# Optimization experiments

Hardware: AMD Instinct MI355X
Metric: run time of the kernel (lower is better)

Reference implementation:

```python
import jax, jax.numpy as jnp
import numpy as np

N = 8192
D = 128
NUM_INSTANCES = 8  # samples per class (balanced PK batch)
ALPHA = 50.0
BASE = 1.0


def setup_inputs() -> dict:
    key = jax.random.key(0)
    k1, = jax.random.split(key, 1)
    x = jax.random.normal(k1, (N, D), dtype=jnp.float32)
    # L2-normalize so pairwise dists ~ sqrt(2) and exp(alpha*(1-d)) stays finite in fp32
    inputs = x / jnp.linalg.norm(x, axis=1, keepdims=True)
    targets = (jnp.arange(N) // NUM_INSTANCES).astype(jnp.int64)
    return {"inputs": inputs, "targets": targets}


def _euclidean_dist(x):
    sq = jnp.sum(x * x, axis=1)  # [n]
    d2 = sq[:, None] + sq[None, :] - 2.0 * (x @ x.T)  # [n, n]
    return jnp.sqrt(jnp.clip(d2, 1e-12, None))


def reference(inputs, targets):
    n = inputs.shape[0]
    dist = _euclidean_dist(inputs)                      # [n, n]
    same = targets[:, None] == targets[None, :]         # [n, n] bool
    eye = jnp.eye(n, dtype=bool)
    pos_mask = same & ~eye                              # positives, excluding self
    neg_mask = ~same                                    # negatives

    e = jnp.exp(ALPHA * (BASE - dist))                  # [n, n]
    pos_logit = jnp.sum(jnp.where(pos_mask, e, 0.0), axis=1)        # [n]
    neg_logit = jnp.sum(jnp.where(neg_mask, e, 0.0), axis=1) * 0.5  # [n]
    loss = jnp.mean(-jnp.log(pos_logit / (pos_logit + neg_logit)))

    pos_d = jnp.sum(jnp.where(pos_mask, dist, 0.0)) / jnp.sum(pos_mask)
    neg_d = jnp.sum(jnp.where(neg_mask, dist, 0.0)) / jnp.sum(neg_mask)
    prec = jnp.float32(1.0)  # err is always 0 in the original code
    return (loss, prec, pos_d, neg_d)
```

## Files before the change

kernel.cpp:

```cpp
#include <hip/hip_runtime.h>

#define NN 8192
#define DD 128
#define C2 72.13475204444817f
#define LN2 0.6931471805599453f
#define NTILE 64
#define NTRI 2080
#define DPAD 2112

typedef __attribute__((ext_vector_type(8))) __bf16 bf16x8;
typedef __attribute__((ext_vector_type(4))) float f32x4;

#if __has_builtin(__builtin_amdgcn_exp2f)
#define EXP2F(x) __builtin_amdgcn_exp2f(x)
#else
#define EXP2F(x) exp2f(x)
#endif
#if __has_builtin(__builtin_amdgcn_sqrtf)
#define SQRTF(x) __builtin_amdgcn_sqrtf(x)
#else
#define SQRTF(x) sqrtf(x)
#endif
#if __has_builtin(__builtin_amdgcn_logf)
#define LOG2F(x) __builtin_amdgcn_logf(x)
#else
#define LOG2F(x) log2f(x)
#endif

__device__ __forceinline__ unsigned short f2bf(float f) {
  unsigned u = __float_as_uint(f);
  u += 0x7FFFu + ((u >> 16) & 1u);
  return (unsigned short)(u >> 16);
}

__device__ __forceinline__ void gload_lds16(const void* g, void* l) {
  __builtin_amdgcn_global_load_lds(
      (const __attribute__((address_space(1))) void*)g,
      (__attribute__((address_space(3))) void*)l, 16, 0, 0);
}

__global__ __launch_bounds__(512) void prep_pos_kernel(
    const float* __restrict__ x, unsigned short* __restrict__ xbf,
    float* __restrict__ sq, float* __restrict__ pos_e,
    float* __restrict__ pos_d, float* __restrict__ dpart,
    float* __restrict__ accs, unsigned* __restrict__ cnt) {
  int w = threadIdx.x >> 6;
  int lane = threadIdx.x & 63;
  int i = blockIdx.x * 8 + w;

  __shared__ float xs[8][128];
  __shared__ float sqs[8];

  const float* xr = x + (size_t)i * DD;
  float a = xr[lane], b = xr[lane + 64];
  xs[w][lane] = a;
  xs[w][lane + 64] = b;

  float s = __fmaf_rn(a, a, b * b);
#pragma unroll
  for (int m = 32; m; m >>= 1) s += __shfl_xor(s, m, 64);
  if (lane == 0) {
    sq[i] = s;
    sqs[w] = s;
  }
  unsigned short* o = xbf + (size_t)i * DD;
  int t1 = lane >> 3, e1 = lane & 7;
  o[((t1 ^ w) << 3) + e1] = f2bf(a);
  o[64 + ((t1 ^ w) << 3) + e1] = f2bf(b);
  if (blockIdx.x == 0) {
    if (threadIdx.x < 32) dpart[NTRI + threadIdx.x] = 0.f;
    if (threadIdx.x == 32) {
      accs[0] = 0.f;
      accs[1] = 0.f;
      accs[2] = 0.f;
    }
    if (threadIdx.x == 33) cnt[0] = 0u;
  }

  __syncthreads();
  float sqi = sqs[w];
  float pe = 0.f, pd = 0.f;
  for (int j = 0; j < 8; ++j) {
    if (j == w) continue;
    float dot = __fmaf_rn(a, xs[j][lane], b * xs[j][lane + 64]);
#pragma unroll
    for (int m = 32; m; m >>= 1) dot += __shfl_xor(dot, m, 64);
    float d2 = fmaxf(__fmaf_rn(-2.f, dot, sqi + sqs[j]), 1e-12f);
    float dist = SQRTF(d2);
    pe += EXP2F(__fmaf_rn(dist, -C2, C2));
    pd += dist;
  }
  if (lane == 0) {
    pos_e[i] = pe;
    pos_d[i] = pd;
  }
}

__global__ __launch_bounds__(256, 2) void tile_kernel(
    const unsigned short* __restrict__ xbf, const float* __restrict__ sq,
    float* __restrict__ part, float* __restrict__ dpart) {
  int lane = threadIdx.x & 63;
  int wave = threadIdx.x >> 6;
  int q = lane >> 4, c = lane & 15;

  int b = blockIdx.x;
  int tr = (int)((129.0f - SQRTF(16641.0f - 8.0f * (float)b)) * 0.5f);
  while (tr > 0 && tr * (129 - tr) / 2 > b) --tr;
  while ((tr + 1) * (128 - tr) / 2 <= b) ++tr;
  int tc = tr + (b - tr * (129 - tr) / 2);
  bool diag = (tr == tc);

  __shared__ char panel[65536];
  __shared__ float rowsum[128];
  __shared__ float colsum[128];
  __shared__ float partd[4];

  {
    const char* gA = (const char*)xbf + (size_t)tr * 32768;
    const char* gB = (const char*)xbf + (size_t)tc * 32768;
    int goff = wave * 1024 + lane * 16;
    char* lA = panel + wave * 1024;
    char* lB = panel + 32768 + wave * 1024;
#pragma unroll
    for (int t = 0; t < 8; ++t) {
      gload_lds16(gA + t * 4096 + goff, lA + t * 4096);
      gload_lds16(gB + t * 4096 + goff, lB + t * 4096);
    }
  }

  if (threadIdx.x < 128)
    rowsum[threadIdx.x] = 0.f;
  else
    colsum[threadIdx.x - 128] = 0.f;

  int I0 = tr * 128 + (wave >> 1) * 64;
  int J0 = tc * 128 + (wave & 1) * 64;

  float sqi[16];
#pragma unroll
  for (int rb = 0; rb < 4; ++rb)
#pragma unroll
    for (int r = 0; r < 4; ++r)
      sqi[rb * 4 + r] = sq[I0 + rb * 16 + q * 4 + r];
  float sqj[4];
#pragma unroll
  for (int cb = 0; cb < 4; ++cb) sqj[cb] = sq[J0 + cb * 16 + c];

  f32x4 acc[4][4];
#pragma unroll
  for (int rb = 0; rb < 4; ++rb)
#pragma unroll
    for (int cb = 0; cb < 4; ++cb) acc[rb][cb] = (f32x4){0.f, 0.f, 0.f, 0.f};

  __syncthreads();

  {
    int swz = (c & 7) << 4;
    const char* pa = panel + (wave >> 1) * 16384 + c * 256;
    const char* pb = panel + 32768 + (wave & 1) * 16384 + c * 256;
#pragma unroll
    for (int ks = 0; ks < 4; ++ks) {
      int koff = (ks * 64 + q * 16) ^ swz;
      bf16x8 ar[4], br[4];
#pragma unroll
      for (int rb = 0; rb < 4; ++rb)
        ar[rb] = *(const bf16x8*)(pa + rb * 4096 + koff);
#pragma unroll
      for (int cb = 0; cb < 4; ++cb)
        br[cb] = *(const bf16x8*)(pb + cb * 4096 + koff);
#pragma unroll
      for (int rb = 0; rb < 4; ++rb)
#pragma unroll
        for (int cb = 0; cb < 4; ++cb)
          acc[rb][cb] = __builtin_amdgcn_mfma_f32_16x16x32_bf16(
              ar[rb], br[cb], acc[rb][cb], 0, 0, 0);
    }
  }

  float tote[16];
#pragma unroll
  for (int k = 0; k < 16; ++k) tote[k] = 0.f;
  float pcol[4] = {0.f, 0.f, 0.f, 0.f};
  float totd = 0.f;

#pragma unroll
  for (int rb = 0; rb < 4; ++rb) {
#pragma unroll
    for (int cb = 0; cb < 4; ++cb) {
      bool diagTile = (I0 + rb * 16) == (J0 + cb * 16);
#pragma unroll
      for (int r = 0; r < 4; ++r) {
        float d2 = fmaxf(
            __fmaf_rn(-2.f, acc[rb][cb][r], sqi[rb * 4 + r] + sqj[cb]),
            1e-12f);
        float dist = SQRTF(d2);
        float ex = EXP2F(__fmaf_rn(dist, -C2, C2));
        if (diagTile && (q * 4 + r) == c) {
          ex = 0.f;
          dist = 0.f;
        }
        tote[rb * 4 + r] += ex;
        pcol[cb] += ex;
        totd += dist;
      }
    }
  }

#pragma unroll
  for (int k = 0; k < 16; ++k) {
    float v = tote[k];
    v += __shfl_xor(v, 1, 64);
    v += __shfl_xor(v, 2, 64);
    v += __shfl_xor(v, 4, 64);
    v += __shfl_xor(v, 8, 64);
    tote[k] = v;
  }
  int woff = (wave >> 1) * 64;
  if (c == 0) {
#pragma unroll
    for (int rb = 0; rb < 4; ++rb)
#pragma unroll
      for (int r = 0; r < 4; ++r)
        atomicAdd(&rowsum[woff + rb * 16 + q * 4 + r], tote[rb * 4 + r]);
  }

  if (!diag) {
    int coff = (wave & 1) * 64;
#pragma unroll
    for (int cb = 0; cb < 4; ++cb) {
      float cs = pcol[cb];
      cs += __shfl_xor(cs, 16, 64);
      cs += __shfl_xor(cs, 32, 64);
      if (q == 0) atomicAdd(&colsum[coff + cb * 16 + c], cs);
    }
  }

#pragma unroll
  for (int m = 32; m; m >>= 1) totd += __shfl_xor(totd, m, 64);
  if (lane == 0) partd[wave] = totd;
  __syncthreads();

  size_t rslot = ((size_t)tr * NTILE + tc) * 128;
  size_t cslot = ((size_t)tc * NTILE + tr) * 128;
  int t = threadIdx.x;
  if (t < 128)
    part[rslot + t] = rowsum[t];
  else if (!diag)
    part[cslot + (t - 128)] = colsum[t - 128];
  if (t == 0) {
    float s = partd[0] + partd[1] + partd[2] + partd[3];
    dpart[blockIdx.x] = diag ? s : 2.f * s;
  }
}

__global__ __launch_bounds__(128) void fin_kernel(
    const float* __restrict__ part, const float* __restrict__ dpart,
    const float* __restrict__ pos_e, const float* __restrict__ pos_d,
    float* accs, unsigned* cnt, float* __restrict__ out) {
  int a = blockIdx.x, c = threadIdx.x;
  const float* pa = part + (size_t)a * NTILE * 128 + c;
  float tot = 0.f;
#pragma unroll
  for (int t = 0; t < 64; ++t) tot += pa[(size_t)t * 128];
  int i = a * 128 + c;
  float p = pos_e[i];
  float denom = __fmaf_rn(0.5f, tot - p, p);
  float lsum = LOG2F(denom) - LOG2F(p);
  float pdsum = pos_d[i];
  float ds = (c < 33) ? dpart[a * 33 + c] : 0.f;

  __shared__ float s1[128], s2[128], s3[128];
  s1[c] = lsum;
  s2[c] = pdsum;
  s3[c] = ds;
  __syncthreads();
  for (int w = 64; w; w >>= 1) {
    if (c < w) {
      s1[c] += s1[c + w];
      s2[c] += s2[c + w];
      s3[c] += s3[c + w];
    }
    __syncthreads();
  }
  if (c == 0) {
    atomicAdd(&accs[0], s1[0]);
    atomicAdd(&accs[1], s2[0]);
    atomicAdd(&accs[2], s3[0]);
    __threadfence();
    unsigned old = atomicAdd(cnt, 1u);
    if (old == 63u) {
      float L = atomicAdd(&accs[0], 0.f);
      float PD = atomicAdd(&accs[1], 0.f);
      float DS = atomicAdd(&accs[2], 0.f);
      out[0] = L * LN2 / (float)NN;
      out[1] = 1.0f;
      out[2] = PD / (float)(NN * 7);
      out[3] = (DS - PD) / ((float)NN * 8184.f);
    }
  }
}

extern "C" void kernel_launch(void* const* d_in, const int* in_sizes, int n_in,
                              void* d_out, int out_size, void* d_ws,
                              size_t ws_size, hipStream_t stream) {
  const float* x = (const float*)d_in[0];
  float* out = (float*)d_out;
  char* ws = (char*)d_ws;

  unsigned short* xbf = (unsigned short*)ws;
  float* sq = (float*)(ws + (size_t)NN * DD * 2);
  float* pos_e = sq + NN;
  float* pos_d = pos_e + NN;
  float* part = pos_d + NN;
  float* dpart = part + (size_t)NTILE * NTILE * 128;
  float* accs = dpart + DPAD;
  unsigned* cnt = (unsigned*)(accs + 3);

  prep_pos_kernel<<<NN / 8, 512, 0, stream>>>(x, xbf, sq, pos_e, pos_d, dpart,
                                              accs, cnt);
  tile_kernel<<<NTRI, 256, 0, stream>>>(xbf, sq, part, dpart);
  fin_kernel<<<64, 128, 0, stream>>>(part, dpart, pos_e, pos_d, accs, cnt,
                                     out);
}
```

Before: 102.9 us.

## Make tile kernel persistent over paired triangle rows with double-buffered B panels

The tile kernel now launches 512 blocks instead of 2080. Each block pairs row p with row 63-p so the triangular work is balanced, keeps both A row panels resident, and loops over a contiguous range of column tiles. It double-buffers the B panel, prefetching the next tile while computing the current one. LDS atomics are replaced by per-wave slots, and the distance partials are accumulated in registers with one dpart per block. This amortises A loads and launch/prologue cost, but uses about 128KB of LDS, so occupancy drops to one block per CU and there are two block barriers per tile.

```diff
diff --git a/kernel.cpp b/kernel.cpp
--- a/kernel.cpp
+++ b/kernel.cpp
@@ -5,8 +5,6 @@
 #define C2 72.13475204444817f
 #define LN2 0.6931471805599453f
 #define NTILE 64
-#define NTRI 2080
-#define DPAD 2112
 
 typedef __attribute__((ext_vector_type(8))) __bf16 bf16x8;
 typedef __attribute__((ext_vector_type(4))) float f32x4;
@@ -42,8 +40,8 @@
 __global__ __launch_bounds__(512) void prep_pos_kernel(
     const float* __restrict__ x, unsigned short* __restrict__ xbf,
     float* __restrict__ sq, float* __restrict__ pos_e,
-    float* __restrict__ pos_d, float* __restrict__ dpart,
-    float* __restrict__ accs, unsigned* __restrict__ cnt) {
+    float* __restrict__ pos_d, float* __restrict__ accs,
+    unsigned* __restrict__ cnt) {
   int w = threadIdx.x >> 6;
   int lane = threadIdx.x & 63;
   int i = blockIdx.x * 8 + w;
@@ -68,13 +66,12 @@
   o[((t1 ^ w) << 3) + e1] = f2bf(a);
   o[64 + ((t1 ^ w) << 3) + e1] = f2bf(b);
   if (blockIdx.x == 0) {
-    if (threadIdx.x < 32) dpart[NTRI + threadIdx.x] = 0.f;
-    if (threadIdx.x == 32) {
+    if (threadIdx.x == 0) {
       accs[0] = 0.f;
       accs[1] = 0.f;
       accs[2] = 0.f;
     }
-    if (threadIdx.x == 33) cnt[0] = 0u;
+    if (threadIdx.x == 1) cnt[0] = 0u;
   }
 
   __syncthreads();
@@ -96,161 +93,179 @@
   }
 }
 
-__global__ __launch_bounds__(256, 2) void tile_kernel(
+__global__ __launch_bounds__(256, 1) void tile_kernel(
     const unsigned short* __restrict__ xbf, const float* __restrict__ sq,
     float* __restrict__ part, float* __restrict__ dpart) {
   int lane = threadIdx.x & 63;
   int wave = threadIdx.x >> 6;
   int q = lane >> 4, c = lane & 15;
-
-  int b = blockIdx.x;
-  int tr = (int)((129.0f - SQRTF(16641.0f - 8.0f * (float)b)) * 0.5f);
-  while (tr > 0 && tr * (129 - tr) / 2 > b) --tr;
-  while ((tr + 1) * (128 - tr) / 2 <= b) ++tr;
-  int tc = tr + (b - tr * (129 - tr) / 2);
-  bool diag = (tr == tc);
-
-  __shared__ char panel[65536];
-  __shared__ float rowsum[128];
-  __shared__ float colsum[128];
+  int p = blockIdx.x >> 4;
+  int s = blockIdx.x & 15;
+  int rA = p, rB = 63 - p;
+  int nA = 64 - p;
+  int k0 = (65 * s) >> 4, k1 = (65 * (s + 1)) >> 4;
+
+  __shared__ char panelA[65536];
+  __shared__ char panelB[65536];
+  __shared__ float rowsumW[4][64];
+  __shared__ float colsumW[4][64];
   __shared__ float partd[4];
 
+  int goff = wave * 1024 + lane * 16;
   {
-    const char* gA = (const char*)xbf + (size_t)tr * 32768;
-    const char* gB = (const char*)xbf + (size_t)tc * 32768;
-    int goff = wave * 1024 + lane * 16;
-    char* lA = panel + wave * 1024;
-    char* lB = panel + 32768 + wave * 1024;
+    const char* gA0 = (const char*)xbf + (size_t)rA * 32768;
+    const char* gA1 = (const char*)xbf + (size_t)rB * 32768;
+    char* lA = panelA + wave * 1024;
 #pragma unroll
     for (int t = 0; t < 8; ++t) {
-      gload_lds16(gA + t * 4096 + goff, lA + t * 4096);
-      gload_lds16(gB + t * 4096 + goff, lB + t * 4096);
-    }
-  }
-
-  if (threadIdx.x < 128)
-    rowsum[threadIdx.x] = 0.f;
-  else
-    colsum[threadIdx.x - 128] = 0.f;
-
-  int I0 = tr * 128 + (wave >> 1) * 64;
-  int J0 = tc * 128 + (wave & 1) * 64;
-
-  float sqi[16];
-#pragma unroll
-  for (int rb = 0; rb < 4; ++rb)
-#pragma unroll
-    for (int r = 0; r < 4; ++r)
-      sqi[rb * 4 + r] = sq[I0 + rb * 16 + q * 4 + r];
-  float sqj[4];
-#pragma unroll
-  for (int cb = 0; cb < 4; ++cb) sqj[cb] = sq[J0 + cb * 16 + c];
-
-  f32x4 acc[4][4];
-#pragma unroll
-  for (int rb = 0; rb < 4; ++rb)
-#pragma unroll
-    for (int cb = 0; cb < 4; ++cb) acc[rb][cb] = (f32x4){0.f, 0.f, 0.f, 0.f};
+      gload_lds16(gA0 + t * 4096 + goff, lA + t * 4096);
+      gload_lds16(gA1 + t * 4096 + goff, lA + 32768 + t * 4096);
+    }
+    int tc0 = (k0 < nA) ? (rA + k0) : (rB + (k0 - nA));
+    const char* gB = (const char*)xbf + (size_t)tc0 * 32768;
+    char* lB = panelB + wave * 1024;
+#pragma unroll
+    for (int t = 0; t < 8; ++t) gload_lds16(gB + t * 4096 + goff, lB + t * 4096);
+  }
+
+  float dacc = 0.f;
+  int swz = (c & 7) << 4;
 
   __syncthreads();
 
-  {
-    int swz = (c & 7) << 4;
-    const char* pa = panel + (wave >> 1) * 16384 + c * 256;
-    const char* pb = panel + 32768 + (wave & 1) * 16384 + c * 256;
-#pragma unroll
-    for (int ks = 0; ks < 4; ++ks) {
-      int koff = (ks * 64 + q * 16) ^ swz;
-      bf16x8 ar[4], br[4];
+  for (int k = k0; k < k1; ++k) {
+    int cur = (k - k0) & 1;
+    if (k + 1 < k1) {
+      int kn = k + 1;
+      int tcn = (kn < nA) ? (rA + kn) : (rB + (kn - nA));
+      const char* gB = (const char*)xbf + (size_t)tcn * 32768;
+      char* lB = panelB + (cur ^ 1) * 32768 + wave * 1024;
+#pragma unroll
+      for (int t = 0; t < 8; ++t)
+        gload_lds16(gB + t * 4096 + goff, lB + t * 4096);
+    }
+    int inB = (k >= nA) ? 1 : 0;
+    int row = inB ? rB : rA;
+    int tc = inB ? (rB + (k - nA)) : (rA + k);
+    bool diag = (row == tc);
+    int I0 = row * 128 + (wave >> 1) * 64;
+    int J0 = tc * 128 + (wave & 1) * 64;
+
+    float sqi[16];
+#pragma unroll
+    for (int rb = 0; rb < 4; ++rb)
+#pragma unroll
+      for (int r = 0; r < 4; ++r)
+        sqi[rb * 4 + r] = sq[I0 + rb * 16 + q * 4 + r];
+    float sqj[4];
+#pragma unroll
+    for (int cb = 0; cb < 4; ++cb) sqj[cb] = sq[J0 + cb * 16 + c];
+
+    f32x4 acc[4][4];
+#pragma unroll
+    for (int rb = 0; rb < 4; ++rb)
+#pragma unroll
+      for (int cb = 0; cb < 4; ++cb)
+        acc[rb][cb] = (f32x4){0.f, 0.f, 0.f, 0.f};
+
+    {
+      const char* pa = panelA + inB * 32768 + (wave >> 1) * 16384 + c * 256;
+      const char* pb = panelB + cur * 32768 + (wave & 1) * 16384 + c * 256;
+#pragma unroll
+      for (int ks = 0; ks < 4; ++ks) {
+        int koff = (ks * 64 + q * 16) ^ swz;
+        bf16x8 ar[4], br[4];
+#pragma unroll
+        for (int rb = 0; rb < 4; ++rb)
+          ar[rb] = *(const bf16x8*)(pa + rb * 4096 + koff);
+#pragma unroll
+        for (int cb = 0; cb < 4; ++cb)
+          br[cb] = *(const bf16x8*)(pb + cb * 4096 + koff);
+#pragma unroll
+        for (int rb = 0; rb < 4; ++rb)
+#pragma unroll
+          for (int cb = 0; cb < 4; ++cb)
+            acc[rb][cb] = __builtin_amdgcn_mfma_f32_16x16x32_bf16(
+                ar[rb], br[cb], acc[rb][cb], 0, 0, 0);
+      }
+    }
+
+    float tote[16];
+#pragma unroll
+    for (int kk = 0; kk < 16; ++kk) tote[kk] = 0.f;
+    float pcol[4] = {0.f, 0.f, 0.f, 0.f};
+    float totd = 0.f;
+
+#pragma unroll
+    for (int rb = 0; rb < 4; ++rb) {
+#pragma unroll
+      for (int cb = 0; cb < 4; ++cb) {
+        bool diagTile = (I0 + rb * 16) == (J0 + cb * 16);
+#pragma unroll
+        for (int r = 0; r < 4; ++r) {
+          float d2 = fmaxf(
+              __fmaf_rn(-2.f, acc[rb][cb][r], sqi[rb * 4 + r] + sqj[cb]),
+              1e-12f);
+          float dist = SQRTF(d2);
+          float ex = EXP2F(__fmaf_rn(dist, -C2, C2));
+          if (diagTile && (q * 4 + r) == c) {
+            ex = 0.f;
+            dist = 0.f;
+          }
+          tote[rb * 4 + r] += ex;
+          pcol[cb] += ex;
+          totd += dist;
+        }
+      }
+    }
+    dacc += diag ? totd : 2.f * totd;
+
+#pragma unroll
+    for (int kk = 0; kk < 16; ++kk) {
+      float v = tote[kk];
+      v += __shfl_xor(v, 1, 64);
+      v += __shfl_xor(v, 2, 64);
+      v += __shfl_xor(v, 4, 64);
+      v += __shfl_xor(v, 8, 64);
+      tote[kk] = v;
+    }
+    if (c == 0) {
 #pragma unroll
       for (int rb = 0; rb < 4; ++rb)
-        ar[rb] = *(const bf16x8*)(pa + rb * 4096 + koff);
-#pragma unroll
-      for (int cb = 0; cb < 4; ++cb)
-        br[cb] = *(const bf16x8*)(pb + cb * 4096 + koff);
-#pragma unroll
-      for (int rb = 0; rb < 4; ++rb)
-#pragma unroll
-        for (int cb = 0; cb < 4; ++cb)
-          acc[rb][cb] = __builtin_amdgcn_mfma_f32_16x16x32_bf16(
-              ar[rb], br[cb], acc[rb][cb], 0, 0, 0);
-    }
-  }
-
-  float tote[16];
-#pragma unroll
-  for (int k = 0; k < 16; ++k) tote[k] = 0.f;
-  float pcol[4] = {0.f, 0.f, 0.f, 0.f};
-  float totd = 0.f;
-
-#pragma unroll
-  for (int rb = 0; rb < 4; ++rb) {
-#pragma unroll
-    for (int cb = 0; cb < 4; ++cb) {
-      bool diagTile = (I0 + rb * 16) == (J0 + cb * 16);
-#pragma unroll
-      for (int r = 0; r < 4; ++r) {
-        float d2 = fmaxf(
-            __fmaf_rn(-2.f, acc[rb][cb][r], sqi[rb * 4 + r] + sqj[cb]),
-            1e-12f);
-        float dist = SQRTF(d2);
-        float ex = EXP2F(__fmaf_rn(dist, -C2, C2));
-        if (diagTile && (q * 4 + r) == c) {
-          ex = 0.f;
-          dist = 0.f;
-        }
-        tote[rb * 4 + r] += ex;
-        pcol[cb] += ex;
-        totd += dist;
-      }
-    }
-  }
-
-#pragma unroll
-  for (int k = 0; k < 16; ++k) {
-    float v = tote[k];
-    v += __shfl_xor(v, 1, 64);
-    v += __shfl_xor(v, 2, 64);
-    v += __shfl_xor(v, 4, 64);
-    v += __shfl_xor(v, 8, 64);
-    tote[k] = v;
-  }
-  int woff = (wave >> 1) * 64;
-  if (c == 0) {
-#pragma unroll
-    for (int rb = 0; rb < 4; ++rb)
-#pragma unroll
-      for (int r = 0; r < 4; ++r)
-        atomicAdd(&rowsum[woff + rb * 16 + q * 4 + r], tote[rb * 4 + r]);
-  }
-
-  if (!diag) {
-    int coff = (wave & 1) * 64;
+#pragma unroll
+        for (int r = 0; r < 4; ++r)
+          rowsumW[wave][rb * 16 + q * 4 + r] = tote[rb * 4 + r];
+    }
 #pragma unroll
     for (int cb = 0; cb < 4; ++cb) {
       float cs = pcol[cb];
       cs += __shfl_xor(cs, 16, 64);
       cs += __shfl_xor(cs, 32, 64);
-      if (q == 0) atomicAdd(&colsum[coff + cb * 16 + c], cs);
-    }
-  }
-
-#pragma unroll
-  for (int m = 32; m; m >>= 1) totd += __shfl_xor(totd, m, 64);
-  if (lane == 0) partd[wave] = totd;
+      if (q == 0) colsumW[wave][cb * 16 + c] = cs;
+    }
+
+    __syncthreads();
+
+    size_t rslot = ((size_t)row * NTILE + tc) * 128;
+    size_t cslot = ((size_t)tc * NTILE + row) * 128;
+    int t = threadIdx.x;
+    if (t < 128) {
+      part[rslot + t] =
+          rowsumW[(t >> 6) * 2][t & 63] + rowsumW[(t >> 6) * 2 + 1][t & 63];
+    } else if (!diag) {
+      int t2 = t - 128;
+      part[cslot + t2] =
+          colsumW[t2 >> 6][t2 & 63] + colsumW[(t2 >> 6) + 2][t2 & 63];
+    }
+    __syncthreads();
+  }
+
+#pragma unroll
+  for (int m = 32; m; m >>= 1) dacc += __shfl_xor(dacc, m, 64);
+  if (lane == 0) partd[wave] = dacc;
   __syncthreads();
-
-  size_t rslot = ((size_t)tr * NTILE + tc) * 128;
-  size_t cslot = ((size_t)tc * NTILE + tr) * 128;
-  int t = threadIdx.x;
-  if (t < 128)
-    part[rslot + t] = rowsum[t];
-  else if (!diag)
-    part[cslot + (t - 128)] = colsum[t - 128];
-  if (t == 0) {
-    float s = partd[0] + partd[1] + partd[2] + partd[3];
-    dpart[blockIdx.x] = diag ? s : 2.f * s;
-  }
+  if (threadIdx.x == 0)
+    dpart[blockIdx.x] = partd[0] + partd[1] + partd[2] + partd[3];
 }
 
 __global__ __launch_bounds__(128) void fin_kernel(
@@ -267,7 +282,7 @@
   float denom = __fmaf_rn(0.5f, tot - p, p);
   float lsum = LOG2F(denom) - LOG2F(p);
   float pdsum = pos_d[i];
-  float ds = (c < 33) ? dpart[a * 33 + c] : 0.f;
+  float ds = (c < 8) ? dpart[a * 8 + c] : 0.f;
 
   __shared__ float s1[128], s2[128], s3[128];
   s1[c] = lsum;
@@ -313,12 +328,12 @@
   float* pos_d = pos_e + NN;
   float* part = pos_d + NN;
   float* dpart = part + (size_t)NTILE * NTILE * 128;
-  float* accs = dpart + DPAD;
+  float* accs = dpart + 512;
   unsigned* cnt = (unsigned*)(accs + 3);
 
-  prep_pos_kernel<<<NN / 8, 512, 0, stream>>>(x, xbf, sq, pos_e, pos_d, dpart,
-                                              accs, cnt);
-  tile_kernel<<<NTRI, 256, 0, stream>>>(xbf, sq, part, dpart);
+  prep_pos_kernel<<<NN / 8, 512, 0, stream>>>(x, xbf, sq, pos_e, pos_d, accs,
+                                              cnt);
+  tile_kernel<<<512, 256, 0, stream>>>(xbf, sq, part, dpart);
   fin_kernel<<<64, 128, 0, stream>>>(part, dpart, pos_e, pos_d, accs, cnt,
                                      out);
 }
```

Measured after the change: 109.7 us. 6.6% more time.
